# Kernel tuning notes

Measured on AMD Instinct MI355X. Metric: run time of the kernel, lower is better.

Reference implementation:

```python
import jax, jax.numpy as jnp
import numpy as np

N, NV, E0, HID, L, H = 32768, 64, 524288, 128, 4, 8
D = HID // H  # 16
SCALE = 1.0 / float(np.sqrt(D))


def _segment_softmax(logits, seg, num_segments):
    # numerically stable softmax grouped by destination node (leading axis = edges)
    m = jax.ops.segment_max(logits, seg, num_segments=num_segments)
    m = jnp.where(jnp.isfinite(m), m, 0.0)  # guard empty segments
    e = jnp.exp(logits - m[seg])
    s = jax.ops.segment_sum(e, seg, num_segments=num_segments)
    return e / (s[seg] + 1e-16)


def _forward(ei0, ei1, x_op, x_v, Wk, bk, Wq, bq, Wv, bv, Wa, ba, skip,
             a_rel, m_rel, p_rel, jk_w_in, jk_b_in, jk_w_out, jk_b_out,
             nm_w0, nm_b0, nm_w1, nm_b1, nm_w2, nm_b2, nm_w3, nm_b3,
             nm_w4, nm_b4, nm_w5, nm_b5, nm_w6, nm_b6,
             gm_w0, gm_b0, gm_w1, gm_b1):
    s0, d0 = ei0[0], ei0[1]
    s1, d1 = ei1[0], ei1[1]
    nm_ws = (nm_w0, nm_w1, nm_w2, nm_w3, nm_w4, nm_w5, nm_w6)
    nm_bs = (nm_b0, nm_b1, nm_b2, nm_b3, nm_b4, nm_b5, nm_b6)
    proj = lambda x, W, b: (x @ W.T + b).reshape(x.shape[0], H, D)
    outs_v = []
    for l in range(L):  # HGTConv layers (node types: 0='op', 1='virtual_op')
        k_op = proj(x_op, Wk[l, 0], bk[l, 0])
        q_op = proj(x_op, Wq[l, 0], bq[l, 0])
        v_op = proj(x_op, Wv[l, 0], bv[l, 0])
        q_v = proj(x_v, Wq[l, 1], bq[l, 1])  # virtual nodes only receive messages
        # relation 0: op -> op
        k0 = jnp.einsum('nhd,hde->nhe', k_op, a_rel[l, 0])
        v0 = jnp.einsum('nhd,hde->nhe', v_op, m_rel[l, 0])
        lg0 = jnp.sum(q_op[d0] * k0[s0], -1) * p_rel[l, 0] * SCALE  # [E0, H]
        al0 = _segment_softmax(lg0, d0, N)
        agg_op = jax.ops.segment_sum(al0[..., None] * v0[s0], d0, num_segments=N).reshape(N, HID)
        # relation 1: op -> virtual_op
        k1 = jnp.einsum('nhd,hde->nhe', k_op, a_rel[l, 1])
        v1 = jnp.einsum('nhd,hde->nhe', v_op, m_rel[l, 1])
        lg1 = jnp.sum(q_v[d1] * k1[s1], -1) * p_rel[l, 1] * SCALE  # [E1, H]
        al1 = _segment_softmax(lg1, d1, NV)
        agg_v = jax.ops.segment_sum(al1[..., None] * v1[s1], d1, num_segments=NV).reshape(NV, HID)
        # target-specific output projection + sigmoid-gated skip (in == out channels)
        o_op = jax.nn.gelu(agg_op, approximate=False) @ Wa[l, 0].T + ba[l, 0]
        g = jax.nn.sigmoid(skip[l, 0])
        x_op = g * o_op + (1.0 - g) * x_op
        o_v = jax.nn.gelu(agg_v, approximate=False) @ Wa[l, 1].T + ba[l, 1]
        g = jax.nn.sigmoid(skip[l, 1])
        x_v = g * o_v + (1.0 - g) * x_v
        outs_v.append(x_v)
    # JK via MultiheadAttention: seq = L layers, batch = NV virtual nodes
    xs = jnp.stack(outs_v)  # [L, NV, HID]
    qkv = xs @ jk_w_in.T + jk_b_in
    q, k, v = jnp.split(qkv, 3, axis=-1)
    q = q.reshape(L, NV, H, D)
    k = k.reshape(L, NV, H, D)
    v = v.reshape(L, NV, H, D)
    attn = jax.nn.softmax(jnp.einsum('qbhd,kbhd->bhqk', q, k) * SCALE, axis=-1)
    o = jnp.einsum('bhqk,kbhd->qbhd', attn, v).reshape(L, NV, HID)
    o = o @ jk_w_out.T + jk_b_out
    h = o.sum(0)  # [NV, HID]; batch_size == NV (1 virtual node per graph)
    for w_, b_ in zip(nm_ws[:-1], nm_bs[:-1]):  # node MLP (GELU hidden layers)
        h = jax.nn.gelu(h @ w_.T + b_, approximate=False)
    h = h @ nm_ws[-1].T + nm_bs[-1]  # [NV, 1]
    h = jax.nn.gelu(h @ gm_w0.T + gm_b0, approximate=False)  # graph MLP
    h = h @ gm_w1.T + gm_b1  # [NV, 1]
    return h[:, 0]  # squeeze(1)


def setup_inputs() -> dict:
    key = jax.random.key(0)
    ks = iter(jax.random.split(key, 64))
    nk = lambda: next(ks)
    w = lambda shape, s: jax.random.normal(nk(), shape, jnp.float32) * s
    inp = {}
    inp['x_op'] = jax.random.normal(nk(), (N, HID), jnp.float32)
    inp['x_v'] = jax.random.normal(nk(), (NV, HID), jnp.float32)
    src0 = jax.random.randint(nk(), (E0,), 0, N, jnp.int32)
    dst0 = jax.random.randint(nk(), (E0,), 0, N, jnp.int32)
    inp['ei0'] = jnp.stack([src0, dst0])
    batch_op = jax.random.randint(nk(), (N,), 0, NV, jnp.int32)  # graph id of each op node
    inp['ei1'] = jnp.stack([jnp.arange(N, dtype=jnp.int32), batch_op])
    for nm in ('Wk', 'Wq', 'Wv', 'Wa'):
        inp[nm] = w((L, 2, HID, HID), 0.1)
    for nm in ('bk', 'bq', 'bv', 'ba'):
        inp[nm] = jnp.zeros((L, 2, HID), jnp.float32)
    inp['skip'] = jnp.ones((L, 2), jnp.float32)
    inp['a_rel'] = w((L, 2, H, D, D), 0.25)
    inp['m_rel'] = w((L, 2, H, D, D), 0.25)
    inp['p_rel'] = jnp.ones((L, 2, H), jnp.float32)
    inp['jk_w_in'] = w((3 * HID, HID), 0.1)
    inp['jk_b_in'] = jnp.zeros((3 * HID,), jnp.float32)
    inp['jk_w_out'] = w((HID, HID), 0.1)
    inp['jk_b_out'] = jnp.zeros((HID,), jnp.float32)
    dims = [128, 64, 32, 16, 8, 4, 2, 1]  # _get_mlp_layer_dims(128, 1) + final out
    for i in range(7):
        inp[f'nm_w{i}'] = w((dims[i + 1], dims[i]), (2.0 / dims[i]) ** 0.5)
        inp[f'nm_b{i}'] = jnp.zeros((dims[i + 1],), jnp.float32)
    inp['gm_w0'] = w((2, 1), 1.0)
    inp['gm_b0'] = jnp.zeros((2,), jnp.float32)
    inp['gm_w1'] = w((1, 2), 0.7)
    inp['gm_b1'] = jnp.zeros((1,), jnp.float32)
    return inp


def reference(x_op, x_v, ei0, ei1, Wk, bk, Wq, bq, Wv, bv, Wa, ba, skip,
              a_rel, m_rel, p_rel, jk_w_in, jk_b_in, jk_w_out, jk_b_out,
              nm_w0, nm_b0, nm_w1, nm_b1, nm_w2, nm_b2, nm_w3, nm_b3,
              nm_w4, nm_b4, nm_w5, nm_b5, nm_w6, nm_b6,
              gm_w0, gm_b0, gm_w1, gm_b1):
    return _forward(ei0, ei1, x_op, x_v, Wk, bk, Wq, bq, Wv, bv, Wa, ba, skip,
                    a_rel, m_rel, p_rel, jk_w_in, jk_b_in, jk_w_out, jk_b_out,
                    nm_w0, nm_b0, nm_w1, nm_b1, nm_w2, nm_b2, nm_w3, nm_b3,
                    nm_w4, nm_b4, nm_w5, nm_b5, nm_w6, nm_b6,
                    gm_w0, gm_b0, gm_w1, gm_b1)
```

## Files before the change

kernel.cpp:

```cpp
#include <hip/hip_runtime.h>

#define NN   32768
#define NV   64
#define E0E  524288
#define HID  128
#define NL   4
#define NH   8
#define DH   16
#define SCALE 0.25f
#define LDA  136
#define CAP0 64
#define CAP1 1024

typedef __attribute__((ext_vector_type(8))) short short8;
typedef __attribute__((ext_vector_type(4))) float f32x4;

__device__ __forceinline__ float gelu_f(float x) {
  return 0.5f * x * (1.0f + erff(x * 0.7071067811865475f));
}
__device__ __forceinline__ float sigmoid_f(float x) {
  return 1.0f / (1.0f + __expf(-x));
}
__device__ __forceinline__ unsigned short f2bf(float x) {
  unsigned u = __float_as_uint(x);
  return (unsigned short)((u + 0x7FFFu + ((u >> 16) & 1u)) >> 16);
}
__device__ __forceinline__ float bf2f(unsigned short h) {
  return __uint_as_float(((unsigned)h) << 16);
}
__device__ __forceinline__ unsigned short f2h(float x) {
  union { _Float16 h; unsigned short u; } cv;
  cv.h = (_Float16)x;
  return cv.u;
}
__device__ __forceinline__ float h2f(unsigned short u) {
  union { _Float16 h; unsigned short u; } cv;
  cv.u = u;
  return (float)cv.h;
}
__device__ __forceinline__ float f16lo(unsigned u) { return h2f((unsigned short)(u & 0xffffu)); }
__device__ __forceinline__ float f16hi(unsigned u) { return h2f((unsigned short)(u >> 16)); }

union SMu {
  struct { unsigned short Ah[64][LDA]; unsigned short Al[64][LDA]; } a;
  struct { float xr[HID]; float xn[HID]; } v;
};

__device__ __forceinline__ void stage_A(unsigned short Ah[][LDA], unsigned short Al[][LDA],
                                        int t, const float* __restrict__ A, int m0, int gelu) {
  #pragma unroll
  for (int i = 0; i < 8; ++i) {
    int idx = t + 256 * i;
    int m = idx >> 5, c4 = (idx & 31) * 4;
    float4 v = *(const float4*)(A + (size_t)(m0 + m) * HID + c4);
    if (gelu) { v.x = gelu_f(v.x); v.y = gelu_f(v.y); v.z = gelu_f(v.z); v.w = gelu_f(v.w); }
    unsigned short h0 = f2bf(v.x), h1 = f2bf(v.y), h2 = f2bf(v.z), h3 = f2bf(v.w);
    *(ushort4*)&Ah[m][c4] = make_ushort4(h0, h1, h2, h3);
    *(ushort4*)&Al[m][c4] = make_ushort4(f2bf(v.x - bf2f(h0)), f2bf(v.y - bf2f(h1)),
                                         f2bf(v.z - bf2f(h2)), f2bf(v.w - bf2f(h3)));
  }
}

__device__ __forceinline__ void mfma_pass(const unsigned short Ah[][LDA],
    const unsigned short Al[][LDA], int t, const unsigned short* __restrict__ Wf,
    f32x4 acc[2][4]) {
  const int w = t >> 6, lane = t & 63, c16 = lane & 15, quad = lane >> 4;
  #pragma unroll
  for (int ks = 0; ks < 4; ++ks) {
    short8 ah[4], al[4];
    #pragma unroll
    for (int s = 0; s < 4; ++s) {
      ah[s] = *(const short8*)&Ah[16 * s + c16][ks * 32 + quad * 8];
      al[s] = *(const short8*)&Al[16 * s + c16][ks * 32 + quad * 8];
    }
    #pragma unroll
    for (int j = 0; j < 2; ++j) {
      const unsigned short* bp = Wf + (size_t)(((2 * w + j) * 4 + ks) * 64 + lane) * 8;
      short8 bh = *(const short8*)bp;
      short8 bl = *(const short8*)(bp + 16384);
      #pragma unroll
      for (int s = 0; s < 4; ++s) {
        acc[j][s] = __builtin_amdgcn_mfma_f32_16x16x32_bf16(ah[s], bh, acc[j][s], 0, 0, 0);
        acc[j][s] = __builtin_amdgcn_mfma_f32_16x16x32_bf16(ah[s], bl, acc[j][s], 0, 0, 0);
        acc[j][s] = __builtin_amdgcn_mfma_f32_16x16x32_bf16(al[s], bh, acc[j][s], 0, 0, 0);
      }
    }
  }
}

__device__ __forceinline__ void proj_q(const unsigned short Ah[][LDA],
    const unsigned short Al[][LDA], int t, int m0,
    const unsigned short* __restrict__ WqF, const float* __restrict__ bq0,
    float* __restrict__ Pq) {
  const int w = t >> 6, c16 = t & 15, quad = (t & 63) >> 4;
  f32x4 acc[2][4] = {};
  mfma_pass(Ah, Al, t, WqF, acc);
  #pragma unroll
  for (int j = 0; j < 2; ++j) {
    const int col = (2 * w + j) * 16 + c16;
    const float bb = bq0[col];
    #pragma unroll
    for (int s = 0; s < 4; ++s)
      #pragma unroll
      for (int r = 0; r < 4; ++r) {
        int m = m0 + 16 * s + quad * 4 + r;
        Pq[(size_t)m * HID + col] = acc[j][s][r] + bb;
      }
  }
}

__device__ __forceinline__ void proj_kv(const unsigned short Ah[][LDA],
    const unsigned short Al[][LDA], int t, int m0,
    const unsigned short* __restrict__ WfK, const float* __restrict__ bK,
    const float* __restrict__ bV, unsigned int* __restrict__ dst) {
  const int w = t >> 6, c16 = t & 15, quad = (t & 63) >> 4;
  unsigned kp[2][4][2];
  {
    f32x4 accK[2][4] = {};
    mfma_pass(Ah, Al, t, WfK, accK);
    #pragma unroll
    for (int j = 0; j < 2; ++j) {
      const float bbk = bK[(2 * w + j) * 16 + c16];
      #pragma unroll
      for (int s = 0; s < 4; ++s)
        #pragma unroll
        for (int rr = 0; rr < 2; ++rr)
          kp[j][s][rr] = (unsigned)f2h(accK[j][s][2 * rr] + bbk)
                       | ((unsigned)f2h(accK[j][s][2 * rr + 1] + bbk) << 16);
    }
  }
  f32x4 accV[2][4] = {};
  mfma_pass(Ah, Al, t, WfK + 32768, accV);
  #pragma unroll
  for (int j = 0; j < 2; ++j) {
    const int col = (2 * w + j) * 16 + c16;
    const float bbv = bV[col];
    #pragma unroll
    for (int s = 0; s < 4; ++s)
      #pragma unroll
      for (int r = 0; r < 4; ++r) {
        int m = m0 + 16 * s + quad * 4 + r;
        unsigned pk = (kp[j][s][r >> 1] >> ((r & 1) * 16)) & 0xffffu;
        unsigned pv = (unsigned)f2h(accV[j][s][r] + bbv);
        dst[(size_t)m * HID + col] = pk | (pv << 16);
      }
  }
}

__global__ __launch_bounds__(256) void k_sf(
    const float* __restrict__ Wk, const float* __restrict__ Wv,
    const float* __restrict__ bk, const float* __restrict__ bv,
    const float* __restrict__ a_rel, const float* __restrict__ m_rel,
    const float* __restrict__ p_rel, const float* __restrict__ Wq,
    const float* __restrict__ Wa, float* __restrict__ CB,
    unsigned short* __restrict__ FW) {
  __shared__ float cwl[HID * HID];
  int m = blockIdx.x, t = threadIdx.x;
  unsigned short* hi = FW + (size_t)m * 32768;
  unsigned short* lo = hi + 16384;
  if (m < 16) {
    int l = m >> 2, mat = m & 3;
    int rel = mat >> 1;
    int isK = ((mat & 1) == 0);
    const float* W  = (isK ? Wk : Wv) + (size_t)(l * 2) * HID * HID;
    const float* bb = (isK ? bk : bv) + (l * 2) * HID;
    const float* R  = (isK ? a_rel : m_rel) + (size_t)((l * 2 + rel) * NH) * DH * DH;
    for (int o = t; o < HID * HID; o += 256) {
      int j = o >> 7, c = o & 127;
      int h = j >> 4, e = j & 15;
      float sc = isK ? (p_rel[(l * 2 + rel) * NH + h] * SCALE) : 1.0f;
      float s = 0.f;
      #pragma unroll
      for (int d = 0; d < DH; ++d)
        s += W[(size_t)(h * DH + d) * HID + c] * R[h * 256 + d * 16 + e];
      cwl[j * HID + c] = s * sc;
    }
    if (t < HID) {
      int j = t, h = j >> 4, e = j & 15;
      float sc = isK ? (p_rel[(l * 2 + rel) * NH + h] * SCALE) : 1.0f;
      float s = 0.f;
      #pragma unroll
      for (int d = 0; d < DH; ++d) s += bb[h * DH + d] * R[h * 256 + d * 16 + e];
      CB[m * HID + j] = s * sc;
    }
    __syncthreads();
    for (int idx = t; idx < 16384; idx += 256) {
      int j = idx & 7, lane = (idx >> 3) & 63, ks = (idx >> 9) & 3, nt = idx >> 11;
      int n = nt * 16 + (lane & 15);
      int k = ks * 32 + (lane >> 4) * 8 + j;
      float x = cwl[n * HID + k];
      unsigned short h = f2bf(x);
      hi[idx] = h;
      lo[idx] = f2bf(x - bf2f(h));
    }
    return;
  }
  const float* src = (m < 20) ? (Wq + (size_t)((m - 16) * 2) * HID * HID)
                              : (Wa + (size_t)((m - 20) * 2) * HID * HID);
  for (int idx = t; idx < 16384; idx += 256) {
    int j = idx & 7, lane = (idx >> 3) & 63, ks = (idx >> 9) & 3, nt = idx >> 11;
    int n = nt * 16 + (lane & 15);
    int k = ks * 32 + (lane >> 4) * 8 + j;
    float x = src[(size_t)n * HID + k];
    unsigned short h = f2bf(x);
    hi[idx] = h;
    lo[idx] = f2bf(x - bf2f(h));
  }
}

struct PreArgs {
  const int *src0, *dst0, *src1, *dst1;
  int *cnt0, *cnt1, *colB0, *colB1;
  const float* x_op; const unsigned short* FW; const float *bq, *CB;
  float* Pq; unsigned int *Pkv0, *Pkv1;
  const float *x_v, *Wq1, *bq1; float* qv;
};

__launch_bounds__(256)
__global__ void k_pre(PreArgs a) {
  __shared__ SMu sm;
  int bx = blockIdx.x, t = threadIdx.x;
  if (bx < E0E / 2048) {
    int base = bx * 2048 + t;
    #pragma unroll
    for (int i = 0; i < 8; ++i) {
      int e = base + i * 256;
      int d = a.dst0[e];
      int pos = atomicAdd(&a.cnt0[d], 1);
      if (pos < CAP0) a.colB0[((size_t)d << 6) + pos] = a.src0[e];
    }
    return;
  }
  bx -= E0E / 2048;
  if (bx < NN / 2048) {
    int base = bx * 2048 + t;
    #pragma unroll
    for (int i = 0; i < 8; ++i) {
      int e = base + i * 256;
      int d = a.dst1[e];
      int pos = atomicAdd(&a.cnt1[d], 1);
      if (pos < CAP1) a.colB1[((size_t)d << 10) + pos] = a.src1[e];
    }
    return;
  }
  bx -= NN / 2048;
  if (bx < 3 * (NN / 64)) {
    int y = bx >> 9, tile = bx & 511;
    int m0 = tile * 64;
    stage_A(sm.a.Ah, sm.a.Al, t, a.x_op, m0, 0);
    __syncthreads();
    if (y == 0)      proj_q (sm.a.Ah, sm.a.Al, t, m0, a.FW + (size_t)16 * 32768, a.bq, a.Pq);
    else if (y == 1) proj_kv(sm.a.Ah, sm.a.Al, t, m0, a.FW, a.CB, a.CB + HID, a.Pkv0);
    else             proj_kv(sm.a.Ah, sm.a.Al, t, m0, a.FW + (size_t)2 * 32768,
                             a.CB + 2 * HID, a.CB + 3 * HID, a.Pkv1);
    return;
  }
  bx -= 3 * (NN / 64);
  if (t < HID) sm.v.xr[t] = a.x_v[bx * HID + t];
  __syncthreads();
  if (t < HID) {
    float s = a.bq1[t];
    const float4* wr = (const float4*)(a.Wq1 + (size_t)t * HID);
    const float4* xx = (const float4*)sm.v.xr;
    #pragma unroll 8
    for (int c = 0; c < HID / 4; ++c) {
      float4 w4 = wr[c], x4 = xx[c];
      s += x4.x * w4.x + x4.y * w4.y + x4.z * w4.z + x4.w * w4.w;
    }
    a.qv[bx * HID + t] = s;
  }
}

__launch_bounds__(256)
__global__ void k_edges(const float* __restrict__ Pq, const unsigned int* __restrict__ Pkv0,
                        const unsigned int* __restrict__ Pkv1,
                        const int* __restrict__ cnt0, const int* __restrict__ colB0,
                        float* __restrict__ agg, const float* __restrict__ qv,
                        const int* __restrict__ cnt1, const int* __restrict__ colB1,
                        float* __restrict__ part, int e0blocks) {
  int lane = threadIdx.x & 63;
  if (blockIdx.x < e0blocks) {
    int n = blockIdx.x * 4 + (threadIdx.x >> 6);
    float2 q = *(const float2*)(Pq + (size_t)n * HID + 2 * lane);
    int cnt = cnt0[n]; if (cnt > CAP0) cnt = CAP0;
    int e = n << 6, e1 = (n << 6) + cnt;
    float acc0 = 0.f, acc1 = 0.f, wsum = 0.f;
    for (; e + 8 <= e1; e += 8) {
      const uint2* r[8];
      #pragma unroll
      for (int u = 0; u < 8; ++u)
        r[u] = (const uint2*)(Pkv0 + ((size_t)colB0[e + u] << 7) + 2 * lane);
      uint2 kv[8];
      #pragma unroll
      for (int u = 0; u < 8; ++u) kv[u] = *r[u];
      float p[8];
      #pragma unroll
      for (int u = 0; u < 8; ++u)
        p[u] = q.x * f16lo(kv[u].x) + q.y * f16lo(kv[u].y);
      #pragma unroll
      for (int u = 0; u < 8; ++u) {
        p[u] += __shfl_xor(p[u], 1); p[u] += __shfl_xor(p[u], 2); p[u] += __shfl_xor(p[u], 4);
      }
      #pragma unroll
      for (int u = 0; u < 8; ++u) {
        float wg = __expf(p[u]);
        wsum += wg; acc0 += wg * f16hi(kv[u].x); acc1 += wg * f16hi(kv[u].y);
      }
    }
    for (; e < e1; ++e) {
      uint2 kv = *(const uint2*)(Pkv0 + ((size_t)colB0[e] << 7) + 2 * lane);
      float p = q.x * f16lo(kv.x) + q.y * f16lo(kv.y);
      p += __shfl_xor(p, 1); p += __shfl_xor(p, 2); p += __shfl_xor(p, 4);
      float wg = __expf(p);
      wsum += wg; acc0 += wg * f16hi(kv.x); acc1 += wg * f16hi(kv.y);
    }
    float inv = 1.0f / (wsum + 1e-16f);
    *(float2*)(agg + (size_t)n * HID + 2 * lane) = make_float2(acc0 * inv, acc1 * inv);
  } else {
    int b2 = blockIdx.x - e0blocks;
    int g = b2 >> 3, ch = b2 & 7;
    int w = threadIdx.x >> 6;
    int slot = ch * 4 + w;
    float2 q = *(const float2*)(qv + g * HID + 2 * lane);
    int tot = cnt1[g]; if (tot > CAP1) tot = CAP1;
    int base = g << 10;
    int len = (tot + 31) >> 5;
    int s0 = base + slot * len;
    int s1 = s0 + len; int lim = base + tot; if (s1 > lim) s1 = lim;
    float acc0 = 0.f, acc1 = 0.f, wsum = 0.f;
    int e = s0;
    for (; e + 4 <= s1; e += 4) {
      uint2 ka = *(const uint2*)(Pkv1 + ((size_t)colB1[e]     << 7) + 2 * lane);
      uint2 kb = *(const uint2*)(Pkv1 + ((size_t)colB1[e + 1] << 7) + 2 * lane);
      uint2 kc = *(const uint2*)(Pkv1 + ((size_t)colB1[e + 2] << 7) + 2 * lane);
      uint2 kd = *(const uint2*)(Pkv1 + ((size_t)colB1[e + 3] << 7) + 2 * lane);
      float pa = q.x * f16lo(ka.x) + q.y * f16lo(ka.y);
      float pb = q.x * f16lo(kb.x) + q.y * f16lo(kb.y);
      float pc = q.x * f16lo(kc.x) + q.y * f16lo(kc.y);
      float pd = q.x * f16lo(kd.x) + q.y * f16lo(kd.y);
      pa += __shfl_xor(pa, 1); pb += __shfl_xor(pb, 1); pc += __shfl_xor(pc, 1); pd += __shfl_xor(pd, 1);
      pa += __shfl_xor(pa, 2); pb += __shfl_xor(pb, 2); pc += __shfl_xor(pc, 2); pd += __shfl_xor(pd, 2);
      pa += __shfl_xor(pa, 4); pb += __shfl_xor(pb, 4); pc += __shfl_xor(pc, 4); pd += __shfl_xor(pd, 4);
      float wa = __expf(pa), wb = __expf(pb), wc = __expf(pc), wd = __expf(pd);
      wsum += (wa + wb) + (wc + wd);
      acc0 += wa * f16hi(ka.x) + wb * f16hi(kb.x) + wc * f16hi(kc.x) + wd * f16hi(kd.x);
      acc1 += wa * f16hi(ka.y) + wb * f16hi(kb.y) + wc * f16hi(kc.y) + wd * f16hi(kd.y);
    }
    for (; e < s1; ++e) {
      uint2 kv = *(const uint2*)(Pkv1 + ((size_t)colB1[e] << 7) + 2 * lane);
      float p = q.x * f16lo(kv.x) + q.y * f16lo(kv.y);
      p += __shfl_xor(p, 1); p += __shfl_xor(p, 2); p += __shfl_xor(p, 4);
      float ww = __expf(p);
      wsum += ww; acc0 += ww * f16hi(kv.x); acc1 += ww * f16hi(kv.y);
    }
    float* pp = part + (size_t)(g * 32 + slot) * 192;
    pp[lane] = acc0; pp[64 + lane] = acc1; pp[128 + lane] = wsum;
  }
}

struct PArgs {
  const float *agg; const unsigned short *WaF_l; const float *ba_l0, *skip_l0, *xold;
  float *xcur;
  const float *part, *Wa_l1, *ba_l1, *skip_l1, *xvold;
  float *xv, *outsv_l, *qv;
  const float *Wq_n1, *bq_n1;
  int do_qv, vonly;
};

__device__ __forceinline__ void vtail(SMu& sm, int t, int v, const PArgs& f) {
  if (t < 64) {
    float a0 = 0.f, a1 = 0.f, ws2 = 0.f;
    for (int s = 0; s < 32; ++s) {
      const float* p = f.part + (size_t)(v * 32 + s) * 192;
      a0 += p[t]; a1 += p[64 + t]; ws2 += p[128 + t];
    }
    float inv = 1.0f / (ws2 + 1e-16f);
    sm.v.xr[2 * t]     = gelu_f(a0 * inv);
    sm.v.xr[2 * t + 1] = gelu_f(a1 * inv);
  }
  __syncthreads();
  if (t < HID) {
    float s = f.ba_l1[t];
    const float4* wr = (const float4*)(f.Wa_l1 + (size_t)t * HID);
    const float4* xx = (const float4*)sm.v.xr;
    #pragma unroll 8
    for (int c = 0; c < HID / 4; ++c) {
      float4 w4 = wr[c], x4 = xx[c];
      s += x4.x * w4.x + x4.y * w4.y + x4.z * w4.z + x4.w * w4.w;
    }
    float gg = sigmoid_f(*f.skip_l1);
    float nv2 = gg * s + (1.f - gg) * f.xvold[v * HID + t];
    f.xv[v * HID + t] = nv2;
    f.outsv_l[v * HID + t] = nv2;
    sm.v.xn[t] = nv2;
  }
  __syncthreads();
  if (f.do_qv && t < HID) {
    float s = f.bq_n1[t];
    const float4* wr = (const float4*)(f.Wq_n1 + (size_t)t * HID);
    const float4* xx = (const float4*)sm.v.xn;
    #pragma unroll 8
    for (int c = 0; c < HID / 4; ++c) {
      float4 w4 = wr[c], x4 = xx[c];
      s += x4.x * w4.x + x4.y * w4.y + x4.z * w4.z + x4.w * w4.w;
    }
    f.qv[v * HID + t] = s;
  }
}

__launch_bounds__(256)
__global__ void k_post_a(PArgs f) {
  __shared__ SMu sm;
  const int t = threadIdx.x;
  int bx = blockIdx.x;
  if (f.vonly) { vtail(sm, t, bx, f); return; }
  if (bx >= NN / 64) { vtail(sm, t, bx - NN / 64, f); return; }
  const int m0 = bx * 64;
  stage_A(sm.a.Ah, sm.a.Al, t, f.agg, m0, 1);
  __syncthreads();
  f32x4 acc[2][4] = {};
  mfma_pass(sm.a.Ah, sm.a.Al, t, f.WaF_l, acc);
  const int w = t >> 6, c16 = t & 15, quad = (t & 63) >> 4;
  float g = sigmoid_f(*f.skip_l0), gm1 = 1.0f - g;
  #pragma unroll
  for (int j = 0; j < 2; ++j) {
    const int col = (2 * w + j) * 16 + c16;
    const float bb = f.ba_l0[col];
    #pragma unroll
    for (int s = 0; s < 4; ++s)
      #pragma unroll
      for (int r = 0; r < 4; ++r) {
        int lm = 16 * s + quad * 4 + r;
        float v = acc[j][s][r] + bb;
        f.xcur[(size_t)(m0 + lm) * HID + col] =
            g * v + gm1 * f.xold[(size_t)(m0 + lm) * HID + col];
      }
  }
}

__launch_bounds__(256)
__global__ void k_post_b(const float* __restrict__ X, const unsigned short* __restrict__ WqF,
                         const unsigned short* __restrict__ CWF,
                         const float* __restrict__ bq0, const float* __restrict__ CBl,
                         float* __restrict__ Pq, unsigned int* __restrict__ Pkv0,
                         unsigned int* __restrict__ Pkv1, int y_base) {
  __shared__ SMu sm;
  const int t = threadIdx.x;
  int y = y_base + (blockIdx.x >> 9), tile = blockIdx.x & 511;
  int m0 = tile * 64;
  stage_A(sm.a.Ah, sm.a.Al, t, X, m0, 0);
  __syncthreads();
  if (y == 0)      proj_q (sm.a.Ah, sm.a.Al, t, m0, WqF, bq0, Pq);
  else if (y == 1) proj_kv(sm.a.Ah, sm.a.Al, t, m0, CWF, CBl, CBl + HID, Pkv0);
  else             proj_kv(sm.a.Ah, sm.a.Al, t, m0, CWF + (size_t)2 * 32768,
                           CBl + 2 * HID, CBl + 3 * HID, Pkv1);
}

struct TailW {
  const float *win, *bin, *wout, *bout;
  const float *nw0, *nb0, *nw1, *nb1, *nw2, *nb2, *nw3, *nb3, *nw4, *nb4, *nw5, *nb5, *nw6, *nb6;
  const float *gw0, *gb0, *gw1, *gb1;
};

__launch_bounds__(128)
__global__ void k_final(const float* __restrict__ outsv, TailW tw, float* __restrict__ outp) {
  __shared__ float xs[4][HID], qq[4][HID], kk[4][HID], vv[4][HID], oo[4][HID];
  __shared__ float att[NH][4][4];
  __shared__ float hb[HID], tb[64];
  int b = blockIdx.x, t = threadIdx.x;
  for (int l = 0; l < 4; ++l) xs[l][t] = outsv[(size_t)(l * NV + b) * HID + t];
  __syncthreads();
  for (int l = 0; l < 4; ++l) {
    float sq = tw.bin[t], sk = tw.bin[t + 128], sv = tw.bin[t + 256];
    const float* wq = tw.win + (size_t)t * HID;
    const float* wk = tw.win + (size_t)(t + 128) * HID;
    const float* wv = tw.win + (size_t)(t + 256) * HID;
    for (int c = 0; c < HID; ++c) {
      float x = xs[l][c];
      sq += x * wq[c]; sk += x * wk[c]; sv += x * wv[c];
    }
    qq[l][t] = sq; kk[l][t] = sk; vv[l][t] = sv;
  }
  __syncthreads();
  {
    int h = t >> 4, ql = (t >> 2) & 3, kl = t & 3;
    float s = 0.f;
    #pragma unroll
    for (int d = 0; d < DH; ++d) s += qq[ql][h * DH + d] * kk[kl][h * DH + d];
    att[h][ql][kl] = s * SCALE;
  }
  __syncthreads();
  if (t < 32) {
    int h = t >> 2, ql = t & 3;
    float m = att[h][ql][0];
    for (int k2 = 1; k2 < 4; ++k2) m = fmaxf(m, att[h][ql][k2]);
    float e[4], s = 0.f;
    for (int k2 = 0; k2 < 4; ++k2) { e[k2] = __expf(att[h][ql][k2] - m); s += e[k2]; }
    for (int k2 = 0; k2 < 4; ++k2) att[h][ql][k2] = e[k2] / s;
  }
  __syncthreads();
  {
    int h = t >> 4;
    #pragma unroll
    for (int ql = 0; ql < 4; ++ql) {
      float s = 0.f;
      #pragma unroll
      for (int kl = 0; kl < 4; ++kl) s += att[h][ql][kl] * vv[kl][t];
      oo[ql][t] = s;
    }
  }
  __syncthreads();
  {
    float s = 0.f;
    const float* wr = tw.wout + (size_t)t * HID;
    for (int l = 0; l < 4; ++l) {
      float ss = tw.bout[t];
      for (int c = 0; c < HID; ++c) ss += oo[l][c] * wr[c];
      s += ss;
    }
    hb[t] = s;
  }
  __syncthreads();
  if (t < 64) { float s = tw.nb0[t]; const float* wr = tw.nw0 + t * 128; for (int c = 0; c < 128; ++c) s += hb[c] * wr[c]; tb[t] = gelu_f(s); }
  __syncthreads();
  if (t < 32) { float s = tw.nb1[t]; const float* wr = tw.nw1 + t * 64;  for (int c = 0; c < 64;  ++c) s += tb[c] * wr[c]; hb[t] = gelu_f(s); }
  __syncthreads();
  if (t < 16) { float s = tw.nb2[t]; const float* wr = tw.nw2 + t * 32;  for (int c = 0; c < 32;  ++c) s += hb[c] * wr[c]; tb[t] = gelu_f(s); }
  __syncthreads();
  if (t < 8)  { float s = tw.nb3[t]; const float* wr = tw.nw3 + t * 16;  for (int c = 0; c < 16;  ++c) s += tb[c] * wr[c]; hb[t] = gelu_f(s); }
  __syncthreads();
  if (t < 4)  { float s = tw.nb4[t]; const float* wr = tw.nw4 + t * 8;   for (int c = 0; c < 8;   ++c) s += hb[c] * wr[c]; tb[t] = gelu_f(s); }
  __syncthreads();
  if (t < 2)  { float s = tw.nb5[t]; const float* wr = tw.nw5 + t * 4;   for (int c = 0; c < 4;   ++c) s += tb[c] * wr[c]; hb[t] = gelu_f(s); }
  __syncthreads();
  if (t == 0) {
    float s = hb[0] * tw.nw6[0] + hb[1] * tw.nw6[1] + tw.nb6[0];
    float g0 = gelu_f(s * tw.gw0[0] + tw.gb0[0]);
    float g1 = gelu_f(s * tw.gw0[1] + tw.gb0[1]);
    outp[b] = g0 * tw.gw1[0] + g1 * tw.gw1[1] + tw.gb1[0];
  }
}

extern "C" void kernel_launch(void* const* d_in, const int* in_sizes, int n_in,
                              void* d_out, int out_size, void* d_ws, size_t ws_size,
                              hipStream_t stream) {
  const float* x_op = (const float*)d_in[0];
  const float* x_v  = (const float*)d_in[1];
  const int*   ei0  = (const int*)d_in[2];
  const int*   ei1  = (const int*)d_in[3];
  const float* Wk   = (const float*)d_in[4];
  const float* Wq   = (const float*)d_in[5];
  const float* Wv   = (const float*)d_in[6];
  const float* Wa   = (const float*)d_in[7];
  const float* bk   = (const float*)d_in[8];
  const float* bq   = (const float*)d_in[9];
  const float* bv   = (const float*)d_in[10];
  const float* ba   = (const float*)d_in[11];
  const float* skip = (const float*)d_in[12];
  const float* a_rel = (const float*)d_in[13];
  const float* m_rel = (const float*)d_in[14];
  const float* p_rel = (const float*)d_in[15];
  (void)in_sizes; (void)n_in; (void)out_size; (void)ws_size;

  char* wsp = (char*)d_ws;
  size_t off = 0;
  auto alloc = [&](size_t bytes) -> void* {
    void* p = wsp + off;
    off += (bytes + 255) & ~(size_t)255;
    return p;
  };
  float* Pq    = (float*)alloc((size_t)NN * HID * 4);
  unsigned int* Pkv0 = (unsigned int*)alloc((size_t)NN * HID * 4);
  unsigned int* Pkv1 = (unsigned int*)alloc((size_t)NN * HID * 4);
  float* xopA  = (float*)alloc((size_t)NN * HID * 4);
  float* xopB  = (float*)alloc((size_t)NN * HID * 4);
  float* agg   = (float*)alloc((size_t)NN * HID * 4);
  float* CB    = (float*)alloc((size_t)16 * HID * 4);
  unsigned short* FW = (unsigned short*)alloc((size_t)24 * 32768 * 2);
  float* xv    = (float*)alloc((size_t)NV * HID * 4);
  float* qv    = (float*)alloc((size_t)NV * HID * 4);
  float* outsv = (float*)alloc((size_t)NL * NV * HID * 4);
  float* part  = (float*)alloc((size_t)NV * 32 * 192 * 4);
  int* cnt0    = (int*)alloc((size_t)NN * 4);
  int* colB0   = (int*)alloc((size_t)NN * CAP0 * 4);
  int* cnt1    = (int*)alloc((size_t)NV * 4);
  int* colB1   = (int*)alloc((size_t)NV * CAP1 * 4);

  hipMemsetAsync(cnt0, 0, (size_t)NN * 4, stream);
  hipMemsetAsync(cnt1, 0, (size_t)NV * 4, stream);

  k_sf<<<24, 256, 0, stream>>>(Wk, Wv, bk, bv, a_rel, m_rel, p_rel, Wq, Wa, CB, FW);

  PreArgs pa;
  pa.src0 = ei0; pa.dst0 = ei0 + E0E;
  pa.src1 = ei1; pa.dst1 = ei1 + NN;
  pa.cnt0 = cnt0; pa.cnt1 = cnt1; pa.colB0 = colB0; pa.colB1 = colB1;
  pa.x_op = x_op; pa.FW = FW; pa.bq = bq; pa.CB = CB;
  pa.Pq = Pq; pa.Pkv0 = Pkv0; pa.Pkv1 = Pkv1;
  pa.x_v = x_v; pa.Wq1 = Wq + (size_t)1 * HID * HID; pa.bq1 = bq + HID; pa.qv = qv;
  k_pre<<<E0E / 2048 + NN / 2048 + 3 * (NN / 64) + NV, 256, 0, stream>>>(pa);

  for (int l = 0; l < NL; ++l) {
    int e0b = (l < NL - 1) ? NN / 4 : 0;
    k_edges<<<e0b + NV * 8, 256, 0, stream>>>(Pq, Pkv0, Pkv1, cnt0, colB0, agg,
                                              qv, cnt1, colB1, part, e0b);
    float* xold = (l == 0) ? (float*)x_op : ((l & 1) ? xopA : xopB);
    float* xcur = (l & 1) ? xopB : xopA;
    PArgs f;
    f.agg = agg;
    f.WaF_l = FW + (size_t)(20 + l) * 32768;
    f.ba_l0 = ba + (l * 2 + 0) * HID;
    f.skip_l0 = skip + l * 2 + 0;
    f.xold = xold;
    f.xcur = xcur;
    f.part = part;
    f.Wa_l1 = Wa + (size_t)(l * 2 + 1) * HID * HID;
    f.ba_l1 = ba + (l * 2 + 1) * HID;
    f.skip_l1 = skip + l * 2 + 1;
    f.xvold = (l == 0) ? x_v : xv;
    f.xv = xv;
    f.outsv_l = outsv + (size_t)l * NV * HID;
    f.qv = qv;
    int ln = (l + 1) & 3;
    f.Wq_n1 = Wq + (size_t)(ln * 2 + 1) * HID * HID;
    f.bq_n1 = bq + (ln * 2 + 1) * HID;
    f.do_qv = (l < NL - 1) ? 1 : 0;
    f.vonly = (l == NL - 1) ? 1 : 0;
    k_post_a<<<(l < NL - 1) ? (NN / 64 + NV) : NV, 256, 0, stream>>>(f);
    if (l < NL - 1) {
      int nsl = (l < 2) ? 3 : 1;
      int yb  = (l < 2) ? 0 : 2;
      k_post_b<<<nsl * (NN / 64), 256, 0, stream>>>(
          xcur, FW + (size_t)(16 + ln) * 32768, FW + (size_t)(ln * 4) * 32768,
          bq + (size_t)ln * 2 * HID, CB + (size_t)ln * 4 * HID, Pq, Pkv0, Pkv1, yb);
    }
  }

  TailW tw;
  tw.win  = (const float*)d_in[16]; tw.bin  = (const float*)d_in[17];
  tw.wout = (const float*)d_in[18]; tw.bout = (const float*)d_in[19];
  tw.nw0 = (const float*)d_in[20]; tw.nb0 = (const float*)d_in[21];
  tw.nw1 = (const float*)d_in[22]; tw.nb1 = (const float*)d_in[23];
  tw.nw2 = (const float*)d_in[24]; tw.nb2 = (const float*)d_in[25];
  tw.nw3 = (const float*)d_in[26]; tw.nb3 = (const float*)d_in[27];
  tw.nw4 = (const float*)d_in[28]; tw.nb4 = (const float*)d_in[29];
  tw.nw5 = (const float*)d_in[30]; tw.nb5 = (const float*)d_in[31];
  tw.nw6 = (const float*)d_in[32]; tw.nb6 = (const float*)d_in[33];
  tw.gw0 = (const float*)d_in[34]; tw.gb0 = (const float*)d_in[35];
  tw.gw1 = (const float*)d_in[36]; tw.gb1 = (const float*)d_in[37];
  k_final<<<NV, 128, 0, stream>>>(outsv, tw, (float*)d_out);
}
```

Before: 560.6 us.

## Fuse final-layer virtual aggregation and tail into one kernel, fold memsets into setup

The last layer's virtual-node edge aggregation, output projection and skip gate are folded into the final JK/MLP tail kernel. This removes two launches, k_edges and a v-only k_post_a, from the last layer. The two counter memsets are replaced by extra blocks in the weight-fold kernel, and the edge-bucketing blocks in k_pre each take twice as many edges. The tail now runs the 1024-edge-per-node virtual aggregation with only 4 waves per node, which may lengthen the serial tail.

```diff
diff --git a/kernel.cpp b/kernel.cpp
--- a/kernel.cpp
+++ b/kernel.cpp
@@ -153,9 +153,15 @@
     const float* __restrict__ a_rel, const float* __restrict__ m_rel,
     const float* __restrict__ p_rel, const float* __restrict__ Wq,
     const float* __restrict__ Wa, float* __restrict__ CB,
-    unsigned short* __restrict__ FW) {
+    unsigned short* __restrict__ FW, int* __restrict__ cnt0, int* __restrict__ cnt1) {
   __shared__ float cwl[HID * HID];
   int m = blockIdx.x, t = threadIdx.x;
+  if (m >= 24) {
+    int i = (m - 24) * 256 + t;
+    cnt0[i] = 0;
+    if (m == 24 && t < NV) cnt1[t] = 0;
+    return;
+  }
   unsigned short* hi = FW + (size_t)m * 32768;
   unsigned short* lo = hi + 16384;
   if (m < 16) {
@@ -220,10 +226,10 @@
 __global__ void k_pre(PreArgs a) {
   __shared__ SMu sm;
   int bx = blockIdx.x, t = threadIdx.x;
-  if (bx < E0E / 2048) {
-    int base = bx * 2048 + t;
-    #pragma unroll
-    for (int i = 0; i < 8; ++i) {
+  if (bx < E0E / 4096) {
+    int base = bx * 4096 + t;
+    #pragma unroll
+    for (int i = 0; i < 16; ++i) {
       int e = base + i * 256;
       int d = a.dst0[e];
       int pos = atomicAdd(&a.cnt0[d], 1);
@@ -231,11 +237,11 @@
     }
     return;
   }
-  bx -= E0E / 2048;
-  if (bx < NN / 2048) {
-    int base = bx * 2048 + t;
-    #pragma unroll
-    for (int i = 0; i < 8; ++i) {
+  bx -= E0E / 4096;
+  if (bx < NN / 4096) {
+    int base = bx * 4096 + t;
+    #pragma unroll
+    for (int i = 0; i < 16; ++i) {
       int e = base + i * 256;
       int d = a.dst1[e];
       int pos = atomicAdd(&a.cnt1[d], 1);
@@ -243,7 +249,7 @@
     }
     return;
   }
-  bx -= NN / 2048;
+  bx -= NN / 4096;
   if (bx < 3 * (NN / 64)) {
     int y = bx >> 9, tile = bx & 511;
     int m0 = tile * 64;
@@ -277,9 +283,9 @@
                         const int* __restrict__ cnt0, const int* __restrict__ colB0,
                         float* __restrict__ agg, const float* __restrict__ qv,
                         const int* __restrict__ cnt1, const int* __restrict__ colB1,
-                        float* __restrict__ part, int e0blocks) {
+                        float* __restrict__ part) {
   int lane = threadIdx.x & 63;
-  if (blockIdx.x < e0blocks) {
+  if (blockIdx.x < NN / 4) {
     int n = blockIdx.x * 4 + (threadIdx.x >> 6);
     float2 q = *(const float2*)(Pq + (size_t)n * HID + 2 * lane);
     int cnt = cnt0[n]; if (cnt > CAP0) cnt = CAP0;
@@ -317,7 +323,7 @@
     float inv = 1.0f / (wsum + 1e-16f);
     *(float2*)(agg + (size_t)n * HID + 2 * lane) = make_float2(acc0 * inv, acc1 * inv);
   } else {
-    int b2 = blockIdx.x - e0blocks;
+    int b2 = blockIdx.x - NN / 4;
     int g = b2 >> 3, ch = b2 & 7;
     int w = threadIdx.x >> 6;
     int slot = ch * 4 + w;
@@ -364,7 +370,7 @@
   const float *part, *Wa_l1, *ba_l1, *skip_l1, *xvold;
   float *xv, *outsv_l, *qv;
   const float *Wq_n1, *bq_n1;
-  int do_qv, vonly;
+  int do_qv;
 };
 
 __device__ __forceinline__ void vtail(SMu& sm, int t, int v, const PArgs& f) {
@@ -413,7 +419,6 @@
   __shared__ SMu sm;
   const int t = threadIdx.x;
   int bx = blockIdx.x;
-  if (f.vonly) { vtail(sm, t, bx, f); return; }
   if (bx >= NN / 64) { vtail(sm, t, bx - NN / 64, f); return; }
   const int m0 = bx * 64;
   stage_A(sm.a.Ah, sm.a.Al, t, f.agg, m0, 1);
@@ -462,27 +467,98 @@
   const float *gw0, *gb0, *gw1, *gb1;
 };
 
-__launch_bounds__(128)
-__global__ void k_final(const float* __restrict__ outsv, TailW tw, float* __restrict__ outp) {
+struct TailArgs {
+  const unsigned int* Pkv1; const int *cnt1, *colB1;
+  const float* qv;
+  const float *Wa_l1, *ba_l1, *skip_l1, *xvold;
+  const float* outsv;
+  TailW tw;
+  float* outp;
+};
+
+__launch_bounds__(256)
+__global__ void k_tail(TailArgs a) {
   __shared__ float xs[4][HID], qq[4][HID], kk[4][HID], vv[4][HID], oo[4][HID];
   __shared__ float att[NH][4][4];
   __shared__ float hb[HID], tb[64];
-  int b = blockIdx.x, t = threadIdx.x;
-  for (int l = 0; l < 4; ++l) xs[l][t] = outsv[(size_t)(l * NV + b) * HID + t];
-  __syncthreads();
-  for (int l = 0; l < 4; ++l) {
-    float sq = tw.bin[t], sk = tw.bin[t + 128], sv = tw.bin[t + 256];
-    const float* wq = tw.win + (size_t)t * HID;
-    const float* wk = tw.win + (size_t)(t + 128) * HID;
-    const float* wv = tw.win + (size_t)(t + 256) * HID;
-    for (int c = 0; c < HID; ++c) {
-      float x = xs[l][c];
-      sq += x * wq[c]; sk += x * wk[c]; sv += x * wv[c];
-    }
-    qq[l][t] = sq; kk[l][t] = sk; vv[l][t] = sv;
-  }
-  __syncthreads();
+  __shared__ float p0[4][64], p1[4][64], pw[4][64];
+  int v = blockIdx.x, t = threadIdx.x;
+  int w = t >> 6, lane = t & 63;
   {
+    float2 q = *(const float2*)(a.qv + v * HID + 2 * lane);
+    int tot = a.cnt1[v]; if (tot > CAP1) tot = CAP1;
+    int base = v << 10;
+    int len = (tot + 3) >> 2;
+    int s0 = base + w * len;
+    int s1 = s0 + len; int lim = base + tot; if (s1 > lim) s1 = lim;
+    float acc0 = 0.f, acc1 = 0.f, wsum = 0.f;
+    int e = s0;
+    for (; e + 4 <= s1; e += 4) {
+      uint2 ka = *(const uint2*)(a.Pkv1 + ((size_t)a.colB1[e]     << 7) + 2 * lane);
+      uint2 kb = *(const uint2*)(a.Pkv1 + ((size_t)a.colB1[e + 1] << 7) + 2 * lane);
+      uint2 kc = *(const uint2*)(a.Pkv1 + ((size_t)a.colB1[e + 2] << 7) + 2 * lane);
+      uint2 kd = *(const uint2*)(a.Pkv1 + ((size_t)a.colB1[e + 3] << 7) + 2 * lane);
+      float pa = q.x * f16lo(ka.x) + q.y * f16lo(ka.y);
+      float pb = q.x * f16lo(kb.x) + q.y * f16lo(kb.y);
+      float pc = q.x * f16lo(kc.x) + q.y * f16lo(kc.y);
+      float pd = q.x * f16lo(kd.x) + q.y * f16lo(kd.y);
+      pa += __shfl_xor(pa, 1); pb += __shfl_xor(pb, 1); pc += __shfl_xor(pc, 1); pd += __shfl_xor(pd, 1);
+      pa += __shfl_xor(pa, 2); pb += __shfl_xor(pb, 2); pc += __shfl_xor(pc, 2); pd += __shfl_xor(pd, 2);
+      pa += __shfl_xor(pa, 4); pb += __shfl_xor(pb, 4); pc += __shfl_xor(pc, 4); pd += __shfl_xor(pd, 4);
+      float wa = __expf(pa), wb = __expf(pb), wc = __expf(pc), wd = __expf(pd);
+      wsum += (wa + wb) + (wc + wd);
+      acc0 += wa * f16hi(ka.x) + wb * f16hi(kb.x) + wc * f16hi(kc.x) + wd * f16hi(kd.x);
+      acc1 += wa * f16hi(ka.y) + wb * f16hi(kb.y) + wc * f16hi(kc.y) + wd * f16hi(kd.y);
+    }
+    for (; e < s1; ++e) {
+      uint2 kv = *(const uint2*)(a.Pkv1 + ((size_t)a.colB1[e] << 7) + 2 * lane);
+      float p = q.x * f16lo(kv.x) + q.y * f16lo(kv.y);
+      p += __shfl_xor(p, 1); p += __shfl_xor(p, 2); p += __shfl_xor(p, 4);
+      float ww = __expf(p);
+      wsum += ww; acc0 += ww * f16hi(kv.x); acc1 += ww * f16hi(kv.y);
+    }
+    p0[w][lane] = acc0; p1[w][lane] = acc1; pw[w][lane] = wsum;
+  }
+  __syncthreads();
+  if (t < 64) {
+    float a0 = p0[0][t] + p0[1][t] + p0[2][t] + p0[3][t];
+    float a1 = p1[0][t] + p1[1][t] + p1[2][t] + p1[3][t];
+    float ws = pw[0][t] + pw[1][t] + pw[2][t] + pw[3][t];
+    float inv = 1.0f / (ws + 1e-16f);
+    hb[2 * t]     = gelu_f(a0 * inv);
+    hb[2 * t + 1] = gelu_f(a1 * inv);
+  }
+  __syncthreads();
+  if (t < HID) {
+    float s = a.ba_l1[t];
+    const float4* wr = (const float4*)(a.Wa_l1 + (size_t)t * HID);
+    const float4* xx = (const float4*)hb;
+    #pragma unroll 8
+    for (int c = 0; c < HID / 4; ++c) {
+      float4 w4 = wr[c], x4 = xx[c];
+      s += x4.x * w4.x + x4.y * w4.y + x4.z * w4.z + x4.w * w4.w;
+    }
+    float gg = sigmoid_f(*a.skip_l1);
+    xs[3][t] = gg * s + (1.f - gg) * a.xvold[v * HID + t];
+    for (int l = 0; l < 3; ++l) xs[l][t] = a.outsv[(size_t)(l * NV + v) * HID + t];
+  }
+  __syncthreads();
+  const TailW& tw = a.tw;
+  if (t < HID) {
+    for (int l = 0; l < 4; ++l) {
+      float sq = tw.bin[t], sk = tw.bin[t + 128], sv = tw.bin[t + 256];
+      const float* wq = tw.win + (size_t)t * HID;
+      const float* wk = tw.win + (size_t)(t + 128) * HID;
+      const float* wv = tw.win + (size_t)(t + 256) * HID;
+      for (int c = 0; c < HID; ++c) {
+        float x = xs[l][c];
+        sq += x * wq[c]; sk += x * wk[c]; sv += x * wv[c];
+      }
+      qq[l][t] = sq; kk[l][t] = sk; vv[l][t] = sv;
+    }
+  }
+  __syncthreads();
+  if (t < 128) {
     int h = t >> 4, ql = (t >> 2) & 3, kl = t & 3;
     float s = 0.f;
     #pragma unroll
@@ -499,7 +575,7 @@
     for (int k2 = 0; k2 < 4; ++k2) att[h][ql][k2] = e[k2] / s;
   }
   __syncthreads();
-  {
+  if (t < 128) {
     int h = t >> 4;
     #pragma unroll
     for (int ql = 0; ql < 4; ++ql) {
@@ -510,7 +586,7 @@
     }
   }
   __syncthreads();
-  {
+  if (t < 128) {
     float s = 0.f;
     const float* wr = tw.wout + (size_t)t * HID;
     for (int l = 0; l < 4; ++l) {
@@ -537,7 +613,7 @@
     float s = hb[0] * tw.nw6[0] + hb[1] * tw.nw6[1] + tw.nb6[0];
     float g0 = gelu_f(s * tw.gw0[0] + tw.gb0[0]);
     float g1 = gelu_f(s * tw.gw0[1] + tw.gb0[1]);
-    outp[b] = g0 * tw.gw1[0] + g1 * tw.gw1[1] + tw.gb1[0];
+    a.outp[v] = g0 * tw.gw1[0] + g1 * tw.gw1[1] + tw.gb1[0];
   }
 }
 
@@ -586,10 +662,8 @@
   int* cnt1    = (int*)alloc((size_t)NV * 4);
   int* colB1   = (int*)alloc((size_t)NV * CAP1 * 4);
 
-  hipMemsetAsync(cnt0, 0, (size_t)NN * 4, stream);
-  hipMemsetAsync(cnt1, 0, (size_t)NV * 4, stream);
-
-  k_sf<<<24, 256, 0, stream>>>(Wk, Wv, bk, bv, a_rel, m_rel, p_rel, Wq, Wa, CB, FW);
+  k_sf<<<24 + NN / 256, 256, 0, stream>>>(Wk, Wv, bk, bv, a_rel, m_rel, p_rel, Wq, Wa,
+                                          CB, FW, cnt0, cnt1);
 
   PreArgs pa;
   pa.src0 = ei0; pa.dst0 = ei0 + E0E;
@@ -598,12 +672,11 @@
   pa.x_op = x_op; pa.FW = FW; pa.bq = bq; pa.CB = CB;
   pa.Pq = Pq; pa.Pkv0 = Pkv0; pa.Pkv1 = Pkv1;
   pa.x_v = x_v; pa.Wq1 = Wq + (size_t)1 * HID * HID; pa.bq1 = bq + HID; pa.qv = qv;
-  k_pre<<<E0E / 2048 + NN / 2048 + 3 * (NN / 64) + NV, 256, 0, stream>>>(pa);
-
-  for (int l = 0; l < NL; ++l) {
-    int e0b = (l < NL - 1) ? NN / 4 : 0;
-    k_edges<<<e0b + NV * 8, 256, 0, stream>>>(Pq, Pkv0, Pkv1, cnt0, colB0, agg,
-                                              qv, cnt1, colB1, part, e0b);
+  k_pre<<<E0E / 4096 + NN / 4096 + 3 * (NN / 64) + NV, 256, 0, stream>>>(pa);
+
+  for (int l = 0; l < NL - 1; ++l) {
+    k_edges<<<NN / 4 + NV * 8, 256, 0, stream>>>(Pq, Pkv0, Pkv1, cnt0, colB0, agg,
+                                                 qv, cnt1, colB1, part);
     float* xold = (l == 0) ? (float*)x_op : ((l & 1) ? xopA : xopB);
     float* xcur = (l & 1) ? xopB : xopA;
     PArgs f;
@@ -621,32 +694,37 @@
     f.xv = xv;
     f.outsv_l = outsv + (size_t)l * NV * HID;
     f.qv = qv;
-    int ln = (l + 1) & 3;
+    int ln = l + 1;
     f.Wq_n1 = Wq + (size_t)(ln * 2 + 1) * HID * HID;
     f.bq_n1 = bq + (ln * 2 + 1) * HID;
-    f.do_qv = (l < NL - 1) ? 1 : 0;
-    f.vonly = (l == NL - 1) ? 1 : 0;
-    k_post_a<<<(l < NL - 1) ? (NN / 64 + NV) : NV, 256, 0, stream>>>(f);
-    if (l < NL - 1) {
-      int nsl = (l < 2) ? 3 : 1;
-      int yb  = (l < 2) ? 0 : 2;
-      k_post_b<<<nsl * (NN / 64), 256, 0, stream>>>(
-          xcur, FW + (size_t)(16 + ln) * 32768, FW + (size_t)(ln * 4) * 32768,
-          bq + (size_t)ln * 2 * HID, CB + (size_t)ln * 4 * HID, Pq, Pkv0, Pkv1, yb);
-    }
-  }
-
-  TailW tw;
-  tw.win  = (const float*)d_in[16]; tw.bin  = (const float*)d_in[17];
-  tw.wout = (const float*)d_in[18]; tw.bout = (const float*)d_in[19];
-  tw.nw0 = (const float*)d_in[20]; tw.nb0 = (const float*)d_in[21];
-  tw.nw1 = (const float*)d_in[22]; tw.nb1 = (const float*)d_in[23];
-  tw.nw2 = (const float*)d_in[24]; tw.nb2 = (const float*)d_in[25];
-  tw.nw3 = (const float*)d_in[26]; tw.nb3 = (const float*)d_in[27];
-  tw.nw4 = (const float*)d_in[28]; tw.nb4 = (const float*)d_in[29];
-  tw.nw5 = (const float*)d_in[30]; tw.nb5 = (const float*)d_in[31];
-  tw.nw6 = (const float*)d_in[32]; tw.nb6 = (const float*)d_in[33];
-  tw.gw0 = (const float*)d_in[34]; tw.gb0 = (const float*)d_in[35];
-  tw.gw1 = (const float*)d_in[36]; tw.gb1 = (const float*)d_in[37];
-  k_final<<<NV, 128, 0, stream>>>(outsv, tw, (float*)d_out);
-}
+    f.do_qv = 1;
+    k_post_a<<<NN / 64 + NV, 256, 0, stream>>>(f);
+    int nsl = (l < 2) ? 3 : 1;
+    int yb  = (l < 2) ? 0 : 2;
+    k_post_b<<<nsl * (NN / 64), 256, 0, stream>>>(
+        xcur, FW + (size_t)(16 + ln) * 32768, FW + (size_t)(ln * 4) * 32768,
+        bq + (size_t)ln * 2 * HID, CB + (size_t)ln * 4 * HID, Pq, Pkv0, Pkv1, yb);
+  }
+
+  TailArgs ta;
+  ta.Pkv1 = Pkv1; ta.cnt1 = cnt1; ta.colB1 = colB1;
+  ta.qv = qv;
+  ta.Wa_l1 = Wa + (size_t)(3 * 2 + 1) * HID * HID;
+  ta.ba_l1 = ba + (3 * 2 + 1) * HID;
+  ta.skip_l1 = skip + 3 * 2 + 1;
+  ta.xvold = xv;
+  ta.outsv = outsv;
+  ta.tw.win  = (const float*)d_in[16]; ta.tw.bin  = (const float*)d_in[17];
+  ta.tw.wout = (const float*)d_in[18]; ta.tw.bout = (const float*)d_in[19];
+  ta.tw.nw0 = (const float*)d_in[20]; ta.tw.nb0 = (const float*)d_in[21];
+  ta.tw.nw1 = (const float*)d_in[22]; ta.tw.nb1 = (const float*)d_in[23];
+  ta.tw.nw2 = (const float*)d_in[24]; ta.tw.nb2 = (const float*)d_in[25];
+  ta.tw.nw3 = (const float*)d_in[26]; ta.tw.nb3 = (const float*)d_in[27];
+  ta.tw.nw4 = (const float*)d_in[28]; ta.tw.nb4 = (const float*)d_in[29];
+  ta.tw.nw5 = (const float*)d_in[30]; ta.tw.nb5 = (const float*)d_in[31];
+  ta.tw.nw6 = (const float*)d_in[32]; ta.tw.nb6 = (const float*)d_in[33];
+  ta.tw.gw0 = (const float*)d_in[34]; ta.tw.gb0 = (const float*)d_in[35];
+  ta.tw.gw1 = (const float*)d_in[36]; ta.tw.gb1 = (const float*)d_in[37];
+  ta.outp = (float*)d_out;
+  k_tail<<<NV, 256, 0, stream>>>(ta);
+}
```

Measured after the change: 556.2 us. Within noise of the previous version (-0.8%).
